# Optimization experiments

Measured on AMD Instinct MI355X. Metric: run time of the kernel, lower is better.

Reference implementation:

```python
import jax, jax.numpy as jnp
import numpy as np

HIDDEN = 1024
HEADS = 16
HEAD_DIM = HIDDEN // HEADS

def setup_inputs() -> dict:
    key = jax.random.key(0)
    ks = jax.random.split(key, 11)
    B, T, D = 2, 2048, HIDDEN
    s = 1.0 / np.sqrt(D)
    return {
        "query": jax.random.normal(ks[0], (B, T, D), jnp.float32),
        "key": jax.random.normal(ks[1], (B, T, D), jnp.float32),
        "value": jax.random.normal(ks[2], (B, T, D), jnp.float32),
        "Wq": jax.random.normal(ks[3], (D, D), jnp.float32) * s,
        "bq": jnp.zeros((D,), jnp.float32),
        "Wk": jax.random.normal(ks[4], (D, D), jnp.float32) * s,
        "bk": jnp.zeros((D,), jnp.float32),
        "Wv": jax.random.normal(ks[5], (D, D), jnp.float32) * s,
        "bv": jnp.zeros((D,), jnp.float32),
        "Wo": jax.random.normal(ks[6], (D, D), jnp.float32) * s,
        "bo": jnp.zeros((D,), jnp.float32),
    }

def reference(query, key, value, Wq, bq, Wk, bk, Wv, bv, Wo, bo):
    B, Tq, D = query.shape
    Tk = key.shape[1]
    H, Hd = HEADS, HEAD_DIM
    # projections -> [B, H, T, Hd]
    Q = (query @ Wq + bq).reshape(B, Tq, H, Hd).transpose(0, 2, 1, 3)
    K = (key @ Wk + bk).reshape(B, Tk, H, Hd).transpose(0, 2, 1, 3)
    V = (value @ Wv + bv).reshape(B, Tk, H, Hd).transpose(0, 2, 1, 3)
    scale = jnp.sqrt(jnp.asarray(Hd, Q.dtype))
    scores = jnp.einsum('bhqd,bhkd->bhqk', Q, K) / scale  # [B,H,Tq,Tk]
    causal = jnp.triu(jnp.ones((Tq, Tk), bool), k=1)
    scores = jnp.where(causal[None, None], jnp.asarray(-jnp.inf, scores.dtype), scores)
    attn = jax.nn.softmax(scores, axis=-1)
    out = jnp.einsum('bhqk,bhkd->bhqd', attn, V)  # [B,H,Tq,Hd]
    out = out.transpose(0, 2, 1, 3).reshape(B, Tq, D)
    return out @ Wo + bo
```

## Files before the change

### kernel.cpp

```cpp
#include <hip/hip_runtime.h>
#include <hip/hip_bf16.h>


typedef __bf16 bf16_t;
typedef __bf16 bf16x8 __attribute__((ext_vector_type(8)));
typedef __bf16 bf16x4 __attribute__((ext_vector_type(4)));
typedef __bf16 bf16x2 __attribute__((ext_vector_type(2)));
typedef short short4v __attribute__((ext_vector_type(4)));
typedef float f32x4 __attribute__((ext_vector_type(4)));
typedef unsigned int u32;

#define D_MODEL 1024
#define SEQ_T   2048
#define NHEAD   16
#define HDIM    64
#define M_ROWS  4096
#define MEGA    (1024 * 1024)

__device__ __forceinline__ void gl2lds16(const void* g, void* l) {
    __builtin_amdgcn_global_load_lds((const __attribute__((address_space(1))) u32*)g,
                                     (__attribute__((address_space(3))) u32*)l, 16, 0, 0);
}

__device__ __forceinline__ short4v as_s4(bf16x4 v) {
    union { bf16x4 h; short4v s; } u; u.h = v; return u.s;
}

__global__ __launch_bounds__(256) void prep(
    const float* __restrict__ Wq, const float* __restrict__ Wk,
    const float* __restrict__ Wv, const float* __restrict__ Wo,
    const float* __restrict__ Xq, const float* __restrict__ Xk, const float* __restrict__ Xv,
    bf16_t* __restrict__ Wqt, bf16_t* __restrict__ Wkt,
    bf16_t* __restrict__ Wvt, bf16_t* __restrict__ Wot,
    bf16_t* __restrict__ Xb)
{
    int blk = blockIdx.x, tid = threadIdx.x;
    if (blk < 4096) {
        int wi = blk >> 10, t = blk & 1023;
        int n0 = (t & 31) * 32, k0 = (t >> 5) * 32;
        const float* W = wi == 0 ? Wq : (wi == 1 ? Wk : (wi == 2 ? Wv : Wo));
        bf16_t* Wt = wi == 0 ? Wqt : (wi == 1 ? Wkt : (wi == 2 ? Wvt : Wot));
        __shared__ float tile[32][33];
        int tx = tid & 31, ty = tid >> 5;
#pragma unroll
        for (int i = 0; i < 32; i += 8)
            tile[ty + i][tx] = W[(k0 + ty + i) * D_MODEL + n0 + tx];
        __syncthreads();
#pragma unroll
        for (int i = 0; i < 32; i += 8)
            Wt[(size_t)(n0 + ty + i) * D_MODEL + k0 + tx] = (bf16_t)tile[tx][ty + i];
    } else {
        int b2 = blk - 4096;
        int xi = b2 >> 10;
        const float* X = xi == 0 ? Xq : (xi == 1 ? Xk : Xv);
        bf16_t* XB = Xb + (size_t)xi * M_ROWS * D_MODEL;
        size_t base = (size_t)(b2 & 1023) * 4096 + tid * 16;
        const float4* xp = (const float4*)(X + base);
        float4 a0 = xp[0], a1 = xp[1], a2 = xp[2], a3 = xp[3];
        bf16x8 o0, o1;
        o0[0] = (bf16_t)a0.x; o0[1] = (bf16_t)a0.y; o0[2] = (bf16_t)a0.z; o0[3] = (bf16_t)a0.w;
        o0[4] = (bf16_t)a1.x; o0[5] = (bf16_t)a1.y; o0[6] = (bf16_t)a1.z; o0[7] = (bf16_t)a1.w;
        o1[0] = (bf16_t)a2.x; o1[1] = (bf16_t)a2.y; o1[2] = (bf16_t)a2.z; o1[3] = (bf16_t)a2.w;
        o1[4] = (bf16_t)a3.x; o1[5] = (bf16_t)a3.y; o1[6] = (bf16_t)a3.z; o1[7] = (bf16_t)a3.w;
        *(bf16x8*)(XB + base) = o0;
        *(bf16x8*)(XB + base + 8) = o1;
    }
}

template <bool PRECAST>
__global__ __launch_bounds__(256) void proj_fused(
    const float* __restrict__ Xq, const float* __restrict__ Xk, const float* __restrict__ Xv,
    const bf16_t* __restrict__ Xb,
    const bf16_t* __restrict__ Wqt, const bf16_t* __restrict__ Wkt, const bf16_t* __restrict__ Wvt,
    const float* __restrict__ bq, const float* __restrict__ bk, const float* __restrict__ bv,
    bf16_t* __restrict__ Qh, bf16_t* __restrict__ Kh, bf16_t* __restrict__ Vt)
{
    __shared__ bf16_t Ab[2][128 * 64];
    __shared__ bf16_t Bb[2][128 * 64];
    int tid = threadIdx.x;
    int w = tid >> 6, lane = tid & 63, lo16 = lane & 15, quad = lane >> 4;
    int m0 = blockIdx.x * 128;
    int proj = blockIdx.y >> 3;
    int n0 = (blockIdx.y & 7) * 128;
    const float*  X    = proj == 0 ? Xq  : (proj == 1 ? Xk  : Xv);
    const bf16_t* XB   = Xb + (size_t)proj * M_ROWS * D_MODEL;
    const bf16_t* Wt   = proj == 0 ? Wqt : (proj == 1 ? Wkt : Wvt);
    const float*  bias = proj == 0 ? bq  : (proj == 1 ? bk  : bv);
    int wm = (w >> 1) * 64, wn = (w & 1) * 64;

    auto stage = [&](int buf, int k0) {
#pragma unroll
        for (int p = 0; p < 4; p++) {
            int idx = p * 256 + tid;
            int row = idx >> 3, cp = idx & 7, cl = (cp - row) & 7;
            if (PRECAST) {
                gl2lds16(XB + (size_t)(m0 + row) * D_MODEL + k0 + cl * 8, Ab[buf] + idx * 8);
            } else {
                const float* as = X + (size_t)(m0 + row) * D_MODEL + k0 + cl * 8;
                float4 a0 = *(const float4*)as, a1 = *(const float4*)(as + 4);
                bf16x8 av;
                av[0] = (bf16_t)a0.x; av[1] = (bf16_t)a0.y; av[2] = (bf16_t)a0.z; av[3] = (bf16_t)a0.w;
                av[4] = (bf16_t)a1.x; av[5] = (bf16_t)a1.y; av[6] = (bf16_t)a1.z; av[7] = (bf16_t)a1.w;
                *(bf16x8*)(Ab[buf] + idx * 8) = av;
            }
            gl2lds16(Wt + (size_t)(n0 + row) * D_MODEL + k0 + cl * 8, Bb[buf] + idx * 8);
        }
    };

    f32x4 acc[4][4];
#pragma unroll
    for (int i = 0; i < 4; i++)
#pragma unroll
        for (int j = 0; j < 4; j++) acc[i][j] = (f32x4){0.f, 0.f, 0.f, 0.f};

    stage(0, 0);
    __syncthreads();
    for (int it = 0; it < 16; it++) {
        int cur = it & 1;
        if (it + 1 < 16) stage(cur ^ 1, (it + 1) * 64);
#pragma unroll
        for (int kh = 0; kh < 2; kh++) {
            bf16x8 af[4], bfr[4];
#pragma unroll
            for (int i = 0; i < 4; i++) {
                int row = wm + i * 16 + lo16;
                af[i] = *(bf16x8*)(Ab[cur] + row * 64 + (((kh * 4 + quad) + row) & 7) * 8);
            }
#pragma unroll
            for (int j = 0; j < 4; j++) {
                int row = wn + j * 16 + lo16;
                bfr[j] = *(bf16x8*)(Bb[cur] + row * 64 + (((kh * 4 + quad) + row) & 7) * 8);
            }
#pragma unroll
            for (int i = 0; i < 4; i++)
#pragma unroll
                for (int j = 0; j < 4; j++)
                    acc[i][j] = __builtin_amdgcn_mfma_f32_16x16x32_bf16(af[i], bfr[j], acc[i][j], 0, 0, 0);
        }
        __syncthreads();
    }

    float qscale = proj == 0 ? 0.125f : 1.0f;
#pragma unroll
    for (int j = 0; j < 4; j++) {
        int col = n0 + wn + j * 16 + lo16;
        float bv2 = bias[col];
        int h = col >> 6, hd = col & 63;
#pragma unroll
        for (int i = 0; i < 4; i++) {
#pragma unroll
            for (int r = 0; r < 4; r++) {
                int m = m0 + wm + i * 16 + quad * 4 + r;
                int b = m >> 11, t = m & 2047;
                bf16_t val = (bf16_t)((acc[i][j][r] + bv2) * qscale);
                if (proj == 2)
                    Vt[(((size_t)(b * NHEAD + h) * HDIM + hd) * SEQ_T) + t] = val;
                else if (proj == 1)
                    Kh[(((size_t)(b * NHEAD + h) * SEQ_T + t) * HDIM) + hd] = val;
                else
                    Qh[(((size_t)(b * NHEAD + h) * SEQ_T + t) * HDIM) + hd] = val;
            }
        }
    }
}

__global__ __launch_bounds__(128) void flash_attn(const bf16_t* __restrict__ Qh,
                                                  const bf16_t* __restrict__ Kh,
                                                  const bf16_t* __restrict__ Vt,
                                                  bf16_t* __restrict__ Ob) {
    int bh = blockIdx.x & 31;
    int pr = blockIdx.x >> 5;
    int tid = threadIdx.x;
    int w = tid >> 6, lane = tid & 63, lo16 = lane & 15, quad = lane >> 4;

    __shared__ bf16_t KL[2][64 * 64];
    __shared__ bf16_t VL[2][64 * 64];

    const bf16_t* Qp = Qh + (size_t)bh * SEQ_T * HDIM;
    const bf16_t* Kp = Kh + (size_t)bh * SEQ_T * HDIM;
    const bf16_t* Vp = Vt + (size_t)bh * HDIM * SEQ_T;
    int b = bh >> 4, h = bh & 15;

    auto stageKV = [&](int buf, int kt) {
#pragma unroll
        for (int p = 0; p < 4; p++) {
            int idx = p * 128 + tid;
            int row = idx >> 3, cp = idx & 7, cl = (cp - row) & 7;
            gl2lds16(Kp + (size_t)(kt * 64 + row) * HDIM + cl * 8, KL[buf] + idx * 8);
            gl2lds16(Vp + (size_t)row * SEQ_T + kt * 64 + cl * 8, VL[buf] + idx * 8);
        }
    };

    int qt_hi = 31 - pr, qt_lo = pr;
    int n0t = qt_hi + 1, ntot = n0t + qt_lo + 1;

    int qt_cur = qt_hi;
    int qbase = qt_cur * 64 + w * 32;
    bf16x8 qf[2][2];
    f32x4 oacc[2][4];
    float lsum[2];

    auto load_q = [&]() {
#pragma unroll
        for (int n = 0; n < 2; n++) {
            const bf16_t* qr = Qp + (size_t)(qbase + n * 16 + lo16) * HDIM;
            qf[n][0] = *(const bf16x8*)(qr + quad * 8);
            qf[n][1] = *(const bf16x8*)(qr + 32 + quad * 8);
        }
    };
    auto zero_state = [&]() {
#pragma unroll
        for (int n = 0; n < 2; n++) {
            lsum[n] = 0.f;
#pragma unroll
            for (int t = 0; t < 4; t++) oacc[n][t] = (f32x4){0.f, 0.f, 0.f, 0.f};
        }
    };
    auto epilogue = [&]() {
#pragma unroll
        for (int n = 0; n < 2; n++) {
            float lt = lsum[n];
            lt += __shfl_xor(lt, 16);
            lt += __shfl_xor(lt, 32);
            float inv = 1.f / lt;
            int q = qbase + n * 16 + lo16;
            bf16_t* dst = Ob + ((size_t)b * SEQ_T + q) * D_MODEL + h * HDIM;
#pragma unroll
            for (int t = 0; t < 4; t++) {
#pragma unroll
                for (int rp = 0; rp < 2; rp++) {
                    int d0 = t * 16 + quad * 4 + rp * 2;
                    bf16x2 pk;
                    pk[0] = (bf16_t)(oacc[n][t][rp * 2] * inv);
                    pk[1] = (bf16_t)(oacc[n][t][rp * 2 + 1] * inv);
                    *(bf16x2*)(dst + d0) = pk;
                }
            }
        }
    };

    load_q();
    zero_state();
    stageKV(0, 0);
    __syncthreads();

    for (int j = 0; j < ntot; j++) {
        int cur = j & 1;
        if (j + 1 < ntot) {
            int jn = j + 1;
            int ktn = jn < n0t ? jn : jn - n0t;
            stageKV(jn & 1, ktn);
        }
        int kt = j < n0t ? j : j - n0t;

        bf16x8 kf[4][2];
#pragma unroll
        for (int s = 0; s < 4; s++) {
            int keyr = s * 16 + lo16;
            kf[s][0] = *(bf16x8*)(KL[cur] + keyr * 64 + ((quad + keyr) & 7) * 8);
            kf[s][1] = *(bf16x8*)(KL[cur] + keyr * 64 + ((quad + 4 + keyr) & 7) * 8);
        }

        bool diag = (kt == qt_cur);
        short4v pf[2][4];
#pragma unroll
        for (int n = 0; n < 2; n++) {
            f32x4 sacc[4];
#pragma unroll
            for (int s = 0; s < 4; s++) sacc[s] = (f32x4){0.f, 0.f, 0.f, 0.f};
#pragma unroll
            for (int s = 0; s < 4; s++) {
                sacc[s] = __builtin_amdgcn_mfma_f32_16x16x32_bf16(kf[s][0], qf[n][0], sacc[s], 0, 0, 0);
                sacc[s] = __builtin_amdgcn_mfma_f32_16x16x32_bf16(kf[s][1], qf[n][1], sacc[s], 0, 0, 0);
            }
            int q = qbase + n * 16 + lo16;
#pragma unroll
            for (int s = 0; s < 4; s++) {
                bf16x4 pv;
#pragma unroll
                for (int r = 0; r < 4; r++) {
                    float e = __expf(sacc[s][r]);
                    if (diag) {
                        int key = kt * 64 + s * 16 + quad * 4 + r;
                        e = (key <= q) ? e : 0.f;
                    }
                    lsum[n] += e;
                    pv[r] = (bf16_t)e;
                }
                pf[n][s] = as_s4(pv);
            }
        }

#pragma unroll
        for (int t = 0; t < 4; t++) {
            int drow = t * 16 + lo16;
#pragma unroll
            for (int s = 0; s < 4; s++) {
                int c = s * 16 + quad * 4;
                int phys = ((c >> 3) + drow) & 7;
                bf16x4 vf = *(bf16x4*)(VL[cur] + drow * 64 + phys * 8 + (c & 7));
                short4v vfs = as_s4(vf);
                oacc[0][t] = __builtin_amdgcn_mfma_f32_16x16x16bf16_1k(vfs, pf[0][s], oacc[0][t], 0, 0, 0);
                oacc[1][t] = __builtin_amdgcn_mfma_f32_16x16x16bf16_1k(vfs, pf[1][s], oacc[1][t], 0, 0, 0);
            }
        }

        __syncthreads();

        if (j == n0t - 1) {
            epilogue();
            qt_cur = qt_lo;
            qbase = qt_cur * 64 + w * 32;
            load_q();
            zero_state();
        }
    }
    epilogue();
}

__global__ __launch_bounds__(256) void out_gemm(const bf16_t* __restrict__ A,
                                                const bf16_t* __restrict__ Wt,
                                                const float* __restrict__ bias,
                                                float* __restrict__ out) {
    __shared__ bf16_t Ab[2][128 * 64];
    __shared__ bf16_t Bb[2][128 * 64];
    int tid = threadIdx.x;
    int w = tid >> 6, lane = tid & 63, lo16 = lane & 15, quad = lane >> 4;
    int m0 = blockIdx.x * 128;
    int n0 = blockIdx.y * 128;
    int wm = (w >> 1) * 64, wn = (w & 1) * 64;

    auto stage = [&](int buf, int k0) {
#pragma unroll
        for (int p = 0; p < 4; p++) {
            int idx = p * 256 + tid;
            int row = idx >> 3, cp = idx & 7, cl = (cp - row) & 7;
            gl2lds16(A  + (size_t)(m0 + row) * D_MODEL + k0 + cl * 8, Ab[buf] + idx * 8);
            gl2lds16(Wt + (size_t)(n0 + row) * D_MODEL + k0 + cl * 8, Bb[buf] + idx * 8);
        }
    };

    f32x4 acc[4][4];
#pragma unroll
    for (int i = 0; i < 4; i++)
#pragma unroll
        for (int j = 0; j < 4; j++) acc[i][j] = (f32x4){0.f, 0.f, 0.f, 0.f};

    stage(0, 0);
    __syncthreads();
    for (int it = 0; it < 16; it++) {
        int cur = it & 1;
        if (it + 1 < 16) stage(cur ^ 1, (it + 1) * 64);
#pragma unroll
        for (int kh = 0; kh < 2; kh++) {
            bf16x8 af[4], bfr[4];
#pragma unroll
            for (int i = 0; i < 4; i++) {
                int row = wm + i * 16 + lo16;
                af[i] = *(bf16x8*)(Ab[cur] + row * 64 + (((kh * 4 + quad) + row) & 7) * 8);
            }
#pragma unroll
            for (int j = 0; j < 4; j++) {
                int row = wn + j * 16 + lo16;
                bfr[j] = *(bf16x8*)(Bb[cur] + row * 64 + (((kh * 4 + quad) + row) & 7) * 8);
            }
#pragma unroll
            for (int i = 0; i < 4; i++)
#pragma unroll
                for (int j = 0; j < 4; j++)
                    acc[i][j] = __builtin_amdgcn_mfma_f32_16x16x32_bf16(af[i], bfr[j], acc[i][j], 0, 0, 0);
        }
        __syncthreads();
    }

#pragma unroll
    for (int j = 0; j < 4; j++) {
        int col = n0 + wn + j * 16 + lo16;
        float bv2 = bias[col];
#pragma unroll
        for (int i = 0; i < 4; i++)
#pragma unroll
            for (int r = 0; r < 4; r++) {
                int m = m0 + wm + i * 16 + quad * 4 + r;
                out[(size_t)m * D_MODEL + col] = acc[i][j][r] + bv2;
            }
    }
}

extern "C" void kernel_launch(void* const* d_in, const int* in_sizes, int n_in,
                              void* d_out, int out_size, void* d_ws, size_t ws_size,
                              hipStream_t stream) {
    const float* q  = (const float*)d_in[0];
    const float* k  = (const float*)d_in[1];
    const float* v  = (const float*)d_in[2];
    const float* Wq = (const float*)d_in[3];
    const float* bq = (const float*)d_in[4];
    const float* Wk = (const float*)d_in[5];
    const float* bk = (const float*)d_in[6];
    const float* Wv = (const float*)d_in[7];
    const float* bv = (const float*)d_in[8];
    const float* Wo = (const float*)d_in[9];
    const float* bo = (const float*)d_in[10];
    float* out = (float*)d_out;

    bf16_t* Wqt = (bf16_t*)d_ws;
    bf16_t* Wkt = Wqt + (size_t)MEGA;
    bf16_t* Wvt = Wkt + (size_t)MEGA;
    bf16_t* Wot = Wvt + (size_t)MEGA;
    bf16_t* Qh  = Wot + (size_t)MEGA;
    bf16_t* Kh  = Qh  + (size_t)M_ROWS * D_MODEL;
    bf16_t* Vt  = Kh  + (size_t)M_ROWS * D_MODEL;
    bf16_t* Xb  = Vt  + (size_t)M_ROWS * D_MODEL;
    bf16_t* Ob  = Xb;

    bool precast = ws_size >= (size_t)(4 * MEGA + 6 * M_ROWS * D_MODEL) * sizeof(bf16_t);

    int prep_blocks = precast ? 4096 + 3 * 1024 : 4096;
    prep<<<prep_blocks, 256, 0, stream>>>(Wq, Wk, Wv, Wo, q, k, v, Wqt, Wkt, Wvt, Wot, Xb);

    dim3 pg(M_ROWS / 128, 24);
    if (precast)
        proj_fused<true><<<pg, 256, 0, stream>>>(q, k, v, Xb, Wqt, Wkt, Wvt, bq, bk, bv, Qh, Kh, Vt);
    else
        proj_fused<false><<<pg, 256, 0, stream>>>(q, k, v, Xb, Wqt, Wkt, Wvt, bq, bk, bv, Qh, Kh, Vt);

    flash_attn<<<32 * 16, 128, 0, stream>>>(Qh, Kh, Vt, Ob);

    dim3 og(M_ROWS / 128, D_MODEL / 128);
    out_gemm<<<og, 256, 0, stream>>>(Ob, Wot, bo, out);
}
```

Baseline: 262.6 us.

## Retile all kernels: bigger prep tiles, single-buffered K32 GEMMs, 4-wave attention

```diff
diff --git a/kernel.cpp b/kernel.cpp
--- a/kernel.cpp
+++ b/kernel.cpp
@@ -35,35 +35,38 @@
     bf16_t* __restrict__ Xb)
 {
     int blk = blockIdx.x, tid = threadIdx.x;
-    if (blk < 4096) {
-        int wi = blk >> 10, t = blk & 1023;
-        int n0 = (t & 31) * 32, k0 = (t >> 5) * 32;
+    if (blk < 1024) {
+        int wi = blk >> 8, t = blk & 255;
+        int n0 = (t & 15) * 64, k0 = (t >> 4) * 64;
         const float* W = wi == 0 ? Wq : (wi == 1 ? Wk : (wi == 2 ? Wv : Wo));
         bf16_t* Wt = wi == 0 ? Wqt : (wi == 1 ? Wkt : (wi == 2 ? Wvt : Wot));
-        __shared__ float tile[32][33];
-        int tx = tid & 31, ty = tid >> 5;
-#pragma unroll
-        for (int i = 0; i < 32; i += 8)
+        __shared__ float tile[64][65];
+        int tx = tid & 63, ty = tid >> 6;
+#pragma unroll
+        for (int i = 0; i < 64; i += 4)
             tile[ty + i][tx] = W[(k0 + ty + i) * D_MODEL + n0 + tx];
         __syncthreads();
 #pragma unroll
-        for (int i = 0; i < 32; i += 8)
+        for (int i = 0; i < 64; i += 4)
             Wt[(size_t)(n0 + ty + i) * D_MODEL + k0 + tx] = (bf16_t)tile[tx][ty + i];
     } else {
-        int b2 = blk - 4096;
-        int xi = b2 >> 10;
+        int b2 = blk - 1024;
+        int xi = b2 >> 9;
         const float* X = xi == 0 ? Xq : (xi == 1 ? Xk : Xv);
         bf16_t* XB = Xb + (size_t)xi * M_ROWS * D_MODEL;
-        size_t base = (size_t)(b2 & 1023) * 4096 + tid * 16;
-        const float4* xp = (const float4*)(X + base);
-        float4 a0 = xp[0], a1 = xp[1], a2 = xp[2], a3 = xp[3];
-        bf16x8 o0, o1;
-        o0[0] = (bf16_t)a0.x; o0[1] = (bf16_t)a0.y; o0[2] = (bf16_t)a0.z; o0[3] = (bf16_t)a0.w;
-        o0[4] = (bf16_t)a1.x; o0[5] = (bf16_t)a1.y; o0[6] = (bf16_t)a1.z; o0[7] = (bf16_t)a1.w;
-        o1[0] = (bf16_t)a2.x; o1[1] = (bf16_t)a2.y; o1[2] = (bf16_t)a2.z; o1[3] = (bf16_t)a2.w;
-        o1[4] = (bf16_t)a3.x; o1[5] = (bf16_t)a3.y; o1[6] = (bf16_t)a3.z; o1[7] = (bf16_t)a3.w;
-        *(bf16x8*)(XB + base) = o0;
-        *(bf16x8*)(XB + base + 8) = o1;
+        size_t base = (size_t)(b2 & 511) * 8192 + tid * 32;
+#pragma unroll
+        for (int half = 0; half < 2; half++) {
+            const float4* xp = (const float4*)(X + base + half * 16);
+            float4 a0 = xp[0], a1 = xp[1], a2 = xp[2], a3 = xp[3];
+            bf16x8 o0, o1;
+            o0[0] = (bf16_t)a0.x; o0[1] = (bf16_t)a0.y; o0[2] = (bf16_t)a0.z; o0[3] = (bf16_t)a0.w;
+            o0[4] = (bf16_t)a1.x; o0[5] = (bf16_t)a1.y; o0[6] = (bf16_t)a1.z; o0[7] = (bf16_t)a1.w;
+            o1[0] = (bf16_t)a2.x; o1[1] = (bf16_t)a2.y; o1[2] = (bf16_t)a2.z; o1[3] = (bf16_t)a2.w;
+            o1[4] = (bf16_t)a3.x; o1[5] = (bf16_t)a3.y; o1[6] = (bf16_t)a3.z; o1[7] = (bf16_t)a3.w;
+            *(bf16x8*)(XB + base + half * 16) = o0;
+            *(bf16x8*)(XB + base + half * 16 + 8) = o1;
+        }
     }
 }
 
@@ -75,8 +78,8 @@
     const float* __restrict__ bq, const float* __restrict__ bk, const float* __restrict__ bv,
     bf16_t* __restrict__ Qh, bf16_t* __restrict__ Kh, bf16_t* __restrict__ Vt)
 {
-    __shared__ bf16_t Ab[2][128 * 64];
-    __shared__ bf16_t Bb[2][128 * 64];
+    __shared__ bf16_t Ab[128 * 32];
+    __shared__ bf16_t Bb[128 * 32];
     int tid = threadIdx.x;
     int w = tid >> 6, lane = tid & 63, lo16 = lane & 15, quad = lane >> 4;
     int m0 = blockIdx.x * 128;
@@ -88,56 +91,47 @@
     const float*  bias = proj == 0 ? bq  : (proj == 1 ? bk  : bv);
     int wm = (w >> 1) * 64, wn = (w & 1) * 64;
 
-    auto stage = [&](int buf, int k0) {
-#pragma unroll
-        for (int p = 0; p < 4; p++) {
+    f32x4 acc[4][4];
+#pragma unroll
+    for (int i = 0; i < 4; i++)
+#pragma unroll
+        for (int j = 0; j < 4; j++) acc[i][j] = (f32x4){0.f, 0.f, 0.f, 0.f};
+
+    for (int k0 = 0; k0 < D_MODEL; k0 += 32) {
+        __syncthreads();
+#pragma unroll
+        for (int p = 0; p < 2; p++) {
             int idx = p * 256 + tid;
-            int row = idx >> 3, cp = idx & 7, cl = (cp - row) & 7;
+            int row = idx >> 2, cp = idx & 3, cl = (cp - row) & 3;
             if (PRECAST) {
-                gl2lds16(XB + (size_t)(m0 + row) * D_MODEL + k0 + cl * 8, Ab[buf] + idx * 8);
+                gl2lds16(XB + (size_t)(m0 + row) * D_MODEL + k0 + cl * 8, Ab + idx * 8);
             } else {
                 const float* as = X + (size_t)(m0 + row) * D_MODEL + k0 + cl * 8;
                 float4 a0 = *(const float4*)as, a1 = *(const float4*)(as + 4);
                 bf16x8 av;
                 av[0] = (bf16_t)a0.x; av[1] = (bf16_t)a0.y; av[2] = (bf16_t)a0.z; av[3] = (bf16_t)a0.w;
                 av[4] = (bf16_t)a1.x; av[5] = (bf16_t)a1.y; av[6] = (bf16_t)a1.z; av[7] = (bf16_t)a1.w;
-                *(bf16x8*)(Ab[buf] + idx * 8) = av;
-            }
-            gl2lds16(Wt + (size_t)(n0 + row) * D_MODEL + k0 + cl * 8, Bb[buf] + idx * 8);
-        }
-    };
-
-    f32x4 acc[4][4];
-#pragma unroll
-    for (int i = 0; i < 4; i++)
-#pragma unroll
-        for (int j = 0; j < 4; j++) acc[i][j] = (f32x4){0.f, 0.f, 0.f, 0.f};
-
-    stage(0, 0);
-    __syncthreads();
-    for (int it = 0; it < 16; it++) {
-        int cur = it & 1;
-        if (it + 1 < 16) stage(cur ^ 1, (it + 1) * 64);
-#pragma unroll
-        for (int kh = 0; kh < 2; kh++) {
-            bf16x8 af[4], bfr[4];
-#pragma unroll
-            for (int i = 0; i < 4; i++) {
-                int row = wm + i * 16 + lo16;
-                af[i] = *(bf16x8*)(Ab[cur] + row * 64 + (((kh * 4 + quad) + row) & 7) * 8);
-            }
-#pragma unroll
-            for (int j = 0; j < 4; j++) {
-                int row = wn + j * 16 + lo16;
-                bfr[j] = *(bf16x8*)(Bb[cur] + row * 64 + (((kh * 4 + quad) + row) & 7) * 8);
-            }
-#pragma unroll
-            for (int i = 0; i < 4; i++)
-#pragma unroll
-                for (int j = 0; j < 4; j++)
-                    acc[i][j] = __builtin_amdgcn_mfma_f32_16x16x32_bf16(af[i], bfr[j], acc[i][j], 0, 0, 0);
-        }
-        __syncthreads();
+                *(bf16x8*)(Ab + idx * 8) = av;
+            }
+            gl2lds16(Wt + (size_t)(n0 + row) * D_MODEL + k0 + cl * 8, Bb + idx * 8);
+        }
+        __syncthreads();
+        bf16x8 af[4], bfr[4];
+#pragma unroll
+        for (int i = 0; i < 4; i++) {
+            int row = wm + i * 16 + lo16;
+            af[i] = *(bf16x8*)(Ab + row * 32 + ((quad + row) & 3) * 8);
+        }
+#pragma unroll
+        for (int j = 0; j < 4; j++) {
+            int row = wn + j * 16 + lo16;
+            bfr[j] = *(bf16x8*)(Bb + row * 32 + ((quad + row) & 3) * 8);
+        }
+#pragma unroll
+        for (int i = 0; i < 4; i++)
+#pragma unroll
+            for (int j = 0; j < 4; j++)
+                acc[i][j] = __builtin_amdgcn_mfma_f32_16x16x32_bf16(af[i], bfr[j], acc[i][j], 0, 0, 0);
     }
 
     float qscale = proj == 0 ? 0.125f : 1.0f;
@@ -164,7 +158,7 @@
     }
 }
 
-__global__ __launch_bounds__(128) void flash_attn(const bf16_t* __restrict__ Qh,
+__global__ __launch_bounds__(256) void flash_attn(const bf16_t* __restrict__ Qh,
                                                   const bf16_t* __restrict__ Kh,
                                                   const bf16_t* __restrict__ Vt,
                                                   bf16_t* __restrict__ Ob) {
@@ -183,8 +177,8 @@
 
     auto stageKV = [&](int buf, int kt) {
 #pragma unroll
-        for (int p = 0; p < 4; p++) {
-            int idx = p * 128 + tid;
+        for (int p = 0; p < 2; p++) {
+            int idx = p * 256 + tid;
             int row = idx >> 3, cp = idx & 7, cl = (cp - row) & 7;
             gl2lds16(Kp + (size_t)(kt * 64 + row) * HDIM + cl * 8, KL[buf] + idx * 8);
             gl2lds16(Vp + (size_t)row * SEQ_T + kt * 64 + cl * 8, VL[buf] + idx * 8);
@@ -195,46 +189,37 @@
     int n0t = qt_hi + 1, ntot = n0t + qt_lo + 1;
 
     int qt_cur = qt_hi;
-    int qbase = qt_cur * 64 + w * 32;
-    bf16x8 qf[2][2];
-    f32x4 oacc[2][4];
-    float lsum[2];
+    int qbase = qt_cur * 64 + w * 16;
+    bf16x8 qf0, qf1;
+    f32x4 oacc[4];
+    float lsum;
 
     auto load_q = [&]() {
-#pragma unroll
-        for (int n = 0; n < 2; n++) {
-            const bf16_t* qr = Qp + (size_t)(qbase + n * 16 + lo16) * HDIM;
-            qf[n][0] = *(const bf16x8*)(qr + quad * 8);
-            qf[n][1] = *(const bf16x8*)(qr + 32 + quad * 8);
-        }
+        const bf16_t* qr = Qp + (size_t)(qbase + lo16) * HDIM;
+        qf0 = *(const bf16x8*)(qr + quad * 8);
+        qf1 = *(const bf16x8*)(qr + 32 + quad * 8);
     };
     auto zero_state = [&]() {
-#pragma unroll
-        for (int n = 0; n < 2; n++) {
-            lsum[n] = 0.f;
-#pragma unroll
-            for (int t = 0; t < 4; t++) oacc[n][t] = (f32x4){0.f, 0.f, 0.f, 0.f};
-        }
+        lsum = 0.f;
+#pragma unroll
+        for (int t = 0; t < 4; t++) oacc[t] = (f32x4){0.f, 0.f, 0.f, 0.f};
     };
     auto epilogue = [&]() {
-#pragma unroll
-        for (int n = 0; n < 2; n++) {
-            float lt = lsum[n];
-            lt += __shfl_xor(lt, 16);
-            lt += __shfl_xor(lt, 32);
-            float inv = 1.f / lt;
-            int q = qbase + n * 16 + lo16;
-            bf16_t* dst = Ob + ((size_t)b * SEQ_T + q) * D_MODEL + h * HDIM;
-#pragma unroll
-            for (int t = 0; t < 4; t++) {
-#pragma unroll
-                for (int rp = 0; rp < 2; rp++) {
-                    int d0 = t * 16 + quad * 4 + rp * 2;
-                    bf16x2 pk;
-                    pk[0] = (bf16_t)(oacc[n][t][rp * 2] * inv);
-                    pk[1] = (bf16_t)(oacc[n][t][rp * 2 + 1] * inv);
-                    *(bf16x2*)(dst + d0) = pk;
-                }
+        float lt = lsum;
+        lt += __shfl_xor(lt, 16);
+        lt += __shfl_xor(lt, 32);
+        float inv = 1.f / lt;
+        int q = qbase + lo16;
+        bf16_t* dst = Ob + ((size_t)b * SEQ_T + q) * D_MODEL + h * HDIM;
+#pragma unroll
+        for (int t = 0; t < 4; t++) {
+#pragma unroll
+            for (int rp = 0; rp < 2; rp++) {
+                int d0 = t * 16 + quad * 4 + rp * 2;
+                bf16x2 pk;
+                pk[0] = (bf16_t)(oacc[t][rp * 2] * inv);
+                pk[1] = (bf16_t)(oacc[t][rp * 2 + 1] * inv);
+                *(bf16x2*)(dst + d0) = pk;
             }
         }
     };
@@ -261,34 +246,32 @@
             kf[s][1] = *(bf16x8*)(KL[cur] + keyr * 64 + ((quad + 4 + keyr) & 7) * 8);
         }
 
+        f32x4 sacc[4];
+#pragma unroll
+        for (int s = 0; s < 4; s++) sacc[s] = (f32x4){0.f, 0.f, 0.f, 0.f};
+#pragma unroll
+        for (int s = 0; s < 4; s++) {
+            sacc[s] = __builtin_amdgcn_mfma_f32_16x16x32_bf16(kf[s][0], qf0, sacc[s], 0, 0, 0);
+            sacc[s] = __builtin_amdgcn_mfma_f32_16x16x32_bf16(kf[s][1], qf1, sacc[s], 0, 0, 0);
+        }
+
         bool diag = (kt == qt_cur);
-        short4v pf[2][4];
-#pragma unroll
-        for (int n = 0; n < 2; n++) {
-            f32x4 sacc[4];
-#pragma unroll
-            for (int s = 0; s < 4; s++) sacc[s] = (f32x4){0.f, 0.f, 0.f, 0.f};
-#pragma unroll
-            for (int s = 0; s < 4; s++) {
-                sacc[s] = __builtin_amdgcn_mfma_f32_16x16x32_bf16(kf[s][0], qf[n][0], sacc[s], 0, 0, 0);
-                sacc[s] = __builtin_amdgcn_mfma_f32_16x16x32_bf16(kf[s][1], qf[n][1], sacc[s], 0, 0, 0);
-            }
-            int q = qbase + n * 16 + lo16;
-#pragma unroll
-            for (int s = 0; s < 4; s++) {
-                bf16x4 pv;
-#pragma unroll
-                for (int r = 0; r < 4; r++) {
-                    float e = __expf(sacc[s][r]);
-                    if (diag) {
-                        int key = kt * 64 + s * 16 + quad * 4 + r;
-                        e = (key <= q) ? e : 0.f;
-                    }
-                    lsum[n] += e;
-                    pv[r] = (bf16_t)e;
+        int q = qbase + lo16;
+        short4v pf[4];
+#pragma unroll
+        for (int s = 0; s < 4; s++) {
+            bf16x4 pv;
+#pragma unroll
+            for (int r = 0; r < 4; r++) {
+                float e = __expf(sacc[s][r]);
+                if (diag) {
+                    int key = kt * 64 + s * 16 + quad * 4 + r;
+                    e = (key <= q) ? e : 0.f;
                 }
-                pf[n][s] = as_s4(pv);
-            }
+                lsum += e;
+                pv[r] = (bf16_t)e;
+            }
+            pf[s] = as_s4(pv);
         }
 
 #pragma unroll
@@ -299,9 +282,7 @@
                 int c = s * 16 + quad * 4;
                 int phys = ((c >> 3) + drow) & 7;
                 bf16x4 vf = *(bf16x4*)(VL[cur] + drow * 64 + phys * 8 + (c & 7));
-                short4v vfs = as_s4(vf);
-                oacc[0][t] = __builtin_amdgcn_mfma_f32_16x16x16bf16_1k(vfs, pf[0][s], oacc[0][t], 0, 0, 0);
-                oacc[1][t] = __builtin_amdgcn_mfma_f32_16x16x16bf16_1k(vfs, pf[1][s], oacc[1][t], 0, 0, 0);
+                oacc[t] = __builtin_amdgcn_mfma_f32_16x16x16bf16_1k(as_s4(vf), pf[s], oacc[t], 0, 0, 0);
             }
         }
 
@@ -310,7 +291,7 @@
         if (j == n0t - 1) {
             epilogue();
             qt_cur = qt_lo;
-            qbase = qt_cur * 64 + w * 32;
+            qbase = qt_cur * 64 + w * 16;
             load_q();
             zero_state();
         }
@@ -322,55 +303,50 @@
                                                 const bf16_t* __restrict__ Wt,
                                                 const float* __restrict__ bias,
                                                 float* __restrict__ out) {
-    __shared__ bf16_t Ab[2][128 * 64];
-    __shared__ bf16_t Bb[2][128 * 64];
+    __shared__ bf16_t Ab[64 * 32];
+    __shared__ bf16_t Bb[128 * 32];
     int tid = threadIdx.x;
     int w = tid >> 6, lane = tid & 63, lo16 = lane & 15, quad = lane >> 4;
-    int m0 = blockIdx.x * 128;
+    int m0 = blockIdx.x * 64;
     int n0 = blockIdx.y * 128;
-    int wm = (w >> 1) * 64, wn = (w & 1) * 64;
-
-    auto stage = [&](int buf, int k0) {
-#pragma unroll
-        for (int p = 0; p < 4; p++) {
+    int wm = (w >> 1) * 32, wn = (w & 1) * 64;
+
+    f32x4 acc[2][4];
+#pragma unroll
+    for (int i = 0; i < 2; i++)
+#pragma unroll
+        for (int j = 0; j < 4; j++) acc[i][j] = (f32x4){0.f, 0.f, 0.f, 0.f};
+
+    for (int k0 = 0; k0 < D_MODEL; k0 += 32) {
+        __syncthreads();
+        {
+            int idx = tid;
+            int row = idx >> 2, cp = idx & 3, cl = (cp - row) & 3;
+            gl2lds16(A + (size_t)(m0 + row) * D_MODEL + k0 + cl * 8, Ab + idx * 8);
+        }
+#pragma unroll
+        for (int p = 0; p < 2; p++) {
             int idx = p * 256 + tid;
-            int row = idx >> 3, cp = idx & 7, cl = (cp - row) & 7;
-            gl2lds16(A  + (size_t)(m0 + row) * D_MODEL + k0 + cl * 8, Ab[buf] + idx * 8);
-            gl2lds16(Wt + (size_t)(n0 + row) * D_MODEL + k0 + cl * 8, Bb[buf] + idx * 8);
-        }
-    };
-
-    f32x4 acc[4][4];
-#pragma unroll
-    for (int i = 0; i < 4; i++)
-#pragma unroll
-        for (int j = 0; j < 4; j++) acc[i][j] = (f32x4){0.f, 0.f, 0.f, 0.f};
-
-    stage(0, 0);
-    __syncthreads();
-    for (int it = 0; it < 16; it++) {
-        int cur = it & 1;
-        if (it + 1 < 16) stage(cur ^ 1, (it + 1) * 64);
-#pragma unroll
-        for (int kh = 0; kh < 2; kh++) {
-            bf16x8 af[4], bfr[4];
-#pragma unroll
-            for (int i = 0; i < 4; i++) {
-                int row = wm + i * 16 + lo16;
-                af[i] = *(bf16x8*)(Ab[cur] + row * 64 + (((kh * 4 + quad) + row) & 7) * 8);
-            }
-#pragma unroll
-            for (int j = 0; j < 4; j++) {
-                int row = wn + j * 16 + lo16;
-                bfr[j] = *(bf16x8*)(Bb[cur] + row * 64 + (((kh * 4 + quad) + row) & 7) * 8);
-            }
-#pragma unroll
-            for (int i = 0; i < 4; i++)
-#pragma unroll
-                for (int j = 0; j < 4; j++)
-                    acc[i][j] = __builtin_amdgcn_mfma_f32_16x16x32_bf16(af[i], bfr[j], acc[i][j], 0, 0, 0);
-        }
-        __syncthreads();
+            int row = idx >> 2, cp = idx & 3, cl = (cp - row) & 3;
+            gl2lds16(Wt + (size_t)(n0 + row) * D_MODEL + k0 + cl * 8, Bb + idx * 8);
+        }
+        __syncthreads();
+        bf16x8 af[2], bfr[4];
+#pragma unroll
+        for (int i = 0; i < 2; i++) {
+            int row = wm + i * 16 + lo16;
+            af[i] = *(bf16x8*)(Ab + row * 32 + ((quad + row) & 3) * 8);
+        }
+#pragma unroll
+        for (int j = 0; j < 4; j++) {
+            int row = wn + j * 16 + lo16;
+            bfr[j] = *(bf16x8*)(Bb + row * 32 + ((quad + row) & 3) * 8);
+        }
+#pragma unroll
+        for (int i = 0; i < 2; i++)
+#pragma unroll
+            for (int j = 0; j < 4; j++)
+                acc[i][j] = __builtin_amdgcn_mfma_f32_16x16x32_bf16(af[i], bfr[j], acc[i][j], 0, 0, 0);
     }
 
 #pragma unroll
@@ -378,7 +354,7 @@
         int col = n0 + wn + j * 16 + lo16;
         float bv2 = bias[col];
 #pragma unroll
-        for (int i = 0; i < 4; i++)
+        for (int i = 0; i < 2; i++)
 #pragma unroll
             for (int r = 0; r < 4; r++) {
                 int m = m0 + wm + i * 16 + quad * 4 + r;
@@ -415,7 +391,7 @@
 
     bool precast = ws_size >= (size_t)(4 * MEGA + 6 * M_ROWS * D_MODEL) * sizeof(bf16_t);
 
-    int prep_blocks = precast ? 4096 + 3 * 1024 : 4096;
+    int prep_blocks = precast ? 1024 + 3 * 512 : 1024;
     prep<<<prep_blocks, 256, 0, stream>>>(Wq, Wk, Wv, Wo, q, k, v, Wqt, Wkt, Wvt, Wot, Xb);
 
     dim3 pg(M_ROWS / 128, 24);
@@ -424,8 +400,8 @@
     else
         proj_fused<false><<<pg, 256, 0, stream>>>(q, k, v, Xb, Wqt, Wkt, Wvt, bq, bk, bv, Qh, Kh, Vt);
 
-    flash_attn<<<32 * 16, 128, 0, stream>>>(Qh, Kh, Vt, Ob);
-
-    dim3 og(M_ROWS / 128, D_MODEL / 128);
+    flash_attn<<<32 * 16, 256, 0, stream>>>(Qh, Kh, Vt, Ob);
+
+    dim3 og(M_ROWS / 64, D_MODEL / 128);
     out_gemm<<<og, 256, 0, stream>>>(Ob, Wot, bo, out);
 }
```

New measurement: 229.6 us. -12.6%, faster.
